# Kernel optimization log

Measured on AMD Instinct MI355X. Metric: run time of the kernel, lower is better.

Reference implementation:

```python
import jax, jax.numpy as jnp
import numpy as np

def setup_inputs() -> dict:
    key = jax.random.key(0)
    k1, k2, k3, k4 = jax.random.split(key, 4)
    B, S, E, H = 4, 4096, 1024, 64
    x = jax.random.normal(k1, (B, S, E), dtype=jnp.float32)
    scale = E ** -0.5  # keep activations well-scaled like trained Linear weights
    Wq = jax.random.normal(k2, (E, H), dtype=jnp.float32) * scale
    Wk = jax.random.normal(k3, (E, H), dtype=jnp.float32) * scale
    Wv = jax.random.normal(k4, (E, H), dtype=jnp.float32) * scale
    return {"x": x, "Wq": Wq, "Wk": Wk, "Wv": Wv}

def reference(x, Wq, Wk, Wv):
    # x: [B, S, E]; W*: [E, H]
    B, S, E = x.shape
    H = Wq.shape[1]
    q = jnp.einsum('bse,eh->bsh', x, Wq)
    k = jnp.einsum('bse,eh->bsh', x, Wk)
    v = jnp.einsum('bse,eh->bsh', x, Wv)
    att = jnp.einsum('bqh,bkh->bqk', q, k) * (H ** -0.5)  # [B, S, S]
    causal = jnp.tril(jnp.ones((S, S), dtype=bool))
    att = jnp.where(causal, att, -jnp.inf)
    att = jax.nn.softmax(att, axis=-1)
    # dropout p=0.0 (eval-mode): identity
    return jnp.einsum('bqk,bkh->bqh', att, v)
```

## Files before the change

kernel.cpp:

```cpp
#include <hip/hip_runtime.h>


using short8 = __attribute__((ext_vector_type(8))) short;
using f32x4  = __attribute__((ext_vector_type(4))) float;

#define MFMA16(A, B, C) __builtin_amdgcn_mfma_f32_16x16x32_bf16((A), (B), (C), 0, 0, 0)

typedef const __attribute__((address_space(1))) void* gas_ptr;
typedef __attribute__((address_space(3))) void*       las_ptr;

__device__ __forceinline__ void gload16(const void* g, void* l) {
    __builtin_amdgcn_global_load_lds((gas_ptr)g, (las_ptr)l, 16, 0, 0);
}

__device__ __forceinline__ unsigned short f2bf(float f) {
    unsigned u = __builtin_bit_cast(unsigned, f);
    u += 0x7fffu + ((u >> 16) & 1u);
    return (unsigned short)(u >> 16);
}
__device__ __forceinline__ float bf2f(unsigned short u) {
    unsigned v = ((unsigned)u) << 16;
    return __builtin_bit_cast(float, v);
}

__device__ __forceinline__ float exp2_fast(float x) {
#if __has_builtin(__builtin_amdgcn_exp2f)
    return __builtin_amdgcn_exp2f(x);
#else
    float r;
    asm("v_exp_f32 %0, %1" : "=v"(r) : "v"(x));
    return r;
#endif
}

__global__ __launch_bounds__(256) void transpose_w(
    const float* __restrict__ Wq,
    const float* __restrict__ Wk,
    const float* __restrict__ Wv,
    unsigned short* __restrict__ Ws)
{
    int o = blockIdx.x * 256 + threadIdx.x;
    if (o < 196608) {
        int j    = o & 7;
        int l    = (o >> 3) & 63;
        int g    = (o >> 9) & 7;
        int rem  = o >> 12;
        int mt   = rem % 3;
        int sk   = rem / 3;
        int c    = g >> 2, nt = g & 3;
        int quad = l >> 4, n  = l & 15;
        int e    = sk * 64 + c * 32 + quad * 8 + j;
        int h    = nt * 16 + n;
        const float* W = (mt == 0) ? Wq : (mt == 1) ? Wk : Wv;
        Ws[o] = f2bf(W[e * 64 + h]);
    }
}

__global__ __launch_bounds__(256, 2) void proj_all(
    const float* __restrict__ x,
    const unsigned short* __restrict__ Ws,
    unsigned short* __restrict__ Qo,
    unsigned short* __restrict__ Ko,
    unsigned short* __restrict__ Vto)
{
    const int m0   = blockIdx.x * 32;
    const int tid  = threadIdx.x;
    const int lane = tid & 63;
    const int wv   = tid >> 6;
    const int rt   = wv & 1;
    const int ch   = wv >> 1;
    const int quad = lane >> 4;
    const int n    = lane & 15;

    __shared__ __align__(16) short wf[2][24][64][8];

    const f32x4 zero4 = {0.f, 0.f, 0.f, 0.f};
    f32x4 acc[3][2];
    #pragma unroll
    for (int mt = 0; mt < 3; ++mt)
        #pragma unroll
        for (int ntl = 0; ntl < 2; ++ntl) acc[mt][ntl] = zero4;

    const float* xrow = x + (size_t)(m0 + rt * 16 + n) * 1024 + 8 * quad;

    auto stageW = [&](int k0, int p) {
        int sk = k0 >> 6;
        #pragma unroll
        for (int it = 0; it < 6; ++it) {
            int f = wv + 4 * it;
            gload16(Ws + (((size_t)sk * 24 + f) << 9) + lane * 8, &wf[p][f][0][0]);
        }
    };

    f32x4 ua[4], ub[4];
    #pragma unroll
    for (int j = 0; j < 4; ++j) {
        const float* s = xrow + ((j & 1) ? 4 : 0) + ((j >> 1) ? 32 : 0);
        ua[j] = *(const f32x4*)s;
    }
    stageW(0, 0);
    __syncthreads();

    auto body = [&](int k0, f32x4 (&uc)[4], f32x4 (&un)[4], int pp) {
        int nk = (k0 < 960) ? k0 + 64 : 0;
        #pragma unroll
        for (int j = 0; j < 4; ++j) {
            const float* s = xrow + nk + ((j & 1) ? 4 : 0) + ((j >> 1) ? 32 : 0);
            un[j] = *(const f32x4*)s;
        }
        if (k0 < 960) stageW(k0 + 64, pp ^ 1);

        short8 a0, a1;
        #pragma unroll
        for (int j = 0; j < 4; ++j) {
            a0[j]     = (short)f2bf(uc[0][j]);
            a0[4 + j] = (short)f2bf(uc[1][j]);
            a1[j]     = (short)f2bf(uc[2][j]);
            a1[4 + j] = (short)f2bf(uc[3][j]);
        }

        #pragma unroll
        for (int mt = 0; mt < 3; ++mt)
            #pragma unroll
            for (int ntl = 0; ntl < 2; ++ntl) {
                int nt = 2 * ch + ntl;
                acc[mt][ntl] = MFMA16(a0, *(const short8*)(&wf[pp][mt * 8 + nt][lane][0]),     acc[mt][ntl]);
                acc[mt][ntl] = MFMA16(a1, *(const short8*)(&wf[pp][mt * 8 + 4 + nt][lane][0]), acc[mt][ntl]);
            }

        __syncthreads();
    };

    for (int k0 = 0; k0 < 1024; k0 += 128) {
        body(k0,      ua, ub, 0);
        body(k0 + 64, ub, ua, 1);
    }

    #pragma unroll
    for (int ntl = 0; ntl < 2; ++ntl) {
        int h = (2 * ch + ntl) * 16 + n;
        #pragma unroll
        for (int r = 0; r < 4; ++r) {
            int m = m0 + rt * 16 + quad * 4 + r;
            Qo[(size_t)m * 64 + h] = f2bf(acc[0][ntl][r]);
            Ko[(size_t)m * 64 + h] = f2bf(acc[1][ntl][r]);
            int b = m >> 12, s2 = m & 4095;
            Vto[((size_t)(b * 80 + h)) * 4096 + s2] = f2bf(acc[2][ntl][r]);
        }
    }
}

template <int SPLIT>
__device__ __forceinline__ void attn_body(
    const unsigned short* __restrict__ Q,
    const unsigned short* __restrict__ K,
    const unsigned short* __restrict__ Vt,
    float* __restrict__ dst,
    int b, int r0, int kt0, int kt1)
{
    const int tid  = threadIdx.x;
    const int lane = tid & 63;
    const int wv   = tid >> 6;
    const int quad = lane >> 4;
    const int n    = lane & 15;
    const int ktmask = r0 >> 6;

    __shared__ __align__(16) short kf[2][8][64][8];
    __shared__ __align__(16) short vf[2][8][64][8];
    __shared__ __align__(16) unsigned short pbuf[4][32][72];

    short8 qa[2][2];
    #pragma unroll
    for (int rg = 0; rg < 2; ++rg) {
        const unsigned short* qp =
            Q + (size_t)(b * 4096 + r0 + wv * 32 + rg * 16 + n) * 64 + quad * 8;
        #pragma unroll
        for (int j = 0; j < 8; ++j) {
            qa[rg][0][j] = (short)f2bf(bf2f(qp[j])      * 0.18033688f);
            qa[rg][1][j] = (short)f2bf(bf2f(qp[32 + j]) * 0.18033688f);
        }
    }

    const f32x4 zero4 = {0.f, 0.f, 0.f, 0.f};
    f32x4 oacc[2][4];
    float lacc[2][4];
    #pragma unroll
    for (int rg = 0; rg < 2; ++rg)
        #pragma unroll
        for (int nt = 0; nt < 4; ++nt) { oacc[rg][nt] = zero4; lacc[rg][nt] = 0.f; }

    const unsigned short* kbase = K  + ((size_t)b * 4096 + n) * 64 + quad * 8;
    const unsigned short* vbase = Vt + ((size_t)b * 80 + n) * 4096 + quad * 8;

    auto stage = [&](int kt, int p) {
        #pragma unroll
        for (int it = 0; it < 4; ++it) {
            int f = wv + 4 * it;
            if (f < 8) {
                int c = f >> 2, nt = f & 3;
                gload16(kbase + (size_t)(kt * 64 + nt * 16) * 64 + c * 32, &kf[p][f][0][0]);
            } else {
                int pnl = f - 8;
                int nt = pnl >> 1, c = pnl & 1;
                gload16(vbase + (size_t)nt * 16 * 4096 + kt * 64 + c * 32, &vf[p][pnl][0][0]);
            }
        }
    };

    int p = 0;
    stage(kt0, 0);
    __syncthreads();

    for (int kt = kt0; kt <= kt1; ++kt) {
        if (kt < kt1) stage(kt + 1, p ^ 1);

        f32x4 sacc[2][4];
        #pragma unroll
        for (int rg = 0; rg < 2; ++rg)
            #pragma unroll
            for (int nt = 0; nt < 4; ++nt) sacc[rg][nt] = zero4;

        __builtin_amdgcn_s_setprio(1);
        #pragma unroll
        for (int nt = 0; nt < 4; ++nt) {
            short8 ka = *(const short8*)(&kf[p][nt][lane][0]);
            short8 kb = *(const short8*)(&kf[p][4 + nt][lane][0]);
            #pragma unroll
            for (int rg = 0; rg < 2; ++rg) {
                sacc[rg][nt] = MFMA16(qa[rg][0], ka, sacc[rg][nt]);
                sacc[rg][nt] = MFMA16(qa[rg][1], kb, sacc[rg][nt]);
            }
        }
        __builtin_amdgcn_s_setprio(0);

        if (kt >= ktmask) {
            #pragma unroll
            for (int rg = 0; rg < 2; ++rg) {
                int qg = r0 + wv * 32 + rg * 16 + quad * 4;
                #pragma unroll
                for (int nt = 0; nt < 4; ++nt)
                    #pragma unroll
                    for (int r = 0; r < 4; ++r) {
                        int key = kt * 64 + nt * 16 + n;
                        if (key > qg + r) sacc[rg][nt][r] = -1e30f;
                    }
            }
        }

        #pragma unroll
        for (int rg = 0; rg < 2; ++rg)
            #pragma unroll
            for (int r = 0; r < 4; ++r) {
                float rs = 0.f;
                #pragma unroll
                for (int nt = 0; nt < 4; ++nt) {
                    unsigned short pv = f2bf(exp2_fast(sacc[rg][nt][r]));
                    pbuf[wv][rg * 16 + quad * 4 + r][nt * 16 + n] = pv;
                    rs += bf2f(pv);
                }
                lacc[rg][r] += rs;
            }

        short8 pa[2][2];
        #pragma unroll
        for (int rg = 0; rg < 2; ++rg) {
            pa[rg][0] = *(const short8*)(&pbuf[wv][rg * 16 + n][quad * 8]);
            pa[rg][1] = *(const short8*)(&pbuf[wv][rg * 16 + n][32 + quad * 8]);
        }
        __builtin_amdgcn_s_setprio(1);
        #pragma unroll
        for (int nt = 0; nt < 4; ++nt) {
            short8 va = *(const short8*)(&vf[p][2 * nt][lane][0]);
            short8 vb = *(const short8*)(&vf[p][2 * nt + 1][lane][0]);
            #pragma unroll
            for (int rg = 0; rg < 2; ++rg) {
                oacc[rg][nt] = MFMA16(pa[rg][0], va, oacc[rg][nt]);
                oacc[rg][nt] = MFMA16(pa[rg][1], vb, oacc[rg][nt]);
            }
        }
        __builtin_amdgcn_s_setprio(0);

        __syncthreads();
        p ^= 1;
    }

    #pragma unroll
    for (int rg = 0; rg < 2; ++rg)
        #pragma unroll
        for (int r = 0; r < 4; ++r) {
            float v = lacc[rg][r];
            v += __shfl_xor(v, 1);
            v += __shfl_xor(v, 2);
            v += __shfl_xor(v, 4);
            v += __shfl_xor(v, 8);
            lacc[rg][r] = v;
        }

    if (SPLIT) {
        #pragma unroll
        for (int rg = 0; rg < 2; ++rg)
            #pragma unroll
            for (int r = 0; r < 4; ++r) {
                int row = wv * 32 + rg * 16 + quad * 4 + r;
                #pragma unroll
                for (int nt = 0; nt < 4; ++nt)
                    dst[row * 64 + nt * 16 + n] = oacc[rg][nt][r];
                if (n == 0) dst[8192 + row] = lacc[rg][r];
            }
    } else {
        #pragma unroll
        for (int rg = 0; rg < 2; ++rg)
            #pragma unroll
            for (int r = 0; r < 4; ++r) {
                float inv = 1.f / lacc[rg][r];
                int q = r0 + wv * 32 + rg * 16 + quad * 4 + r;
                #pragma unroll
                for (int nt = 0; nt < 4; ++nt)
                    dst[(size_t)(b * 4096 + q) * 64 + nt * 16 + n] = oacc[rg][nt][r] * inv;
            }
    }
}

__global__ __launch_bounds__(256, 3) void attn_part(
    const unsigned short* __restrict__ Q,
    const unsigned short* __restrict__ K,
    const unsigned short* __restrict__ Vt,
    float* __restrict__ Part)
{
    int id = blockIdx.x;
    int b  = id & 3;
    int t  = 143 - (id >> 2);
    int g  = 0;
    while (2 * (g + 1) * (g + 2) <= t) ++g;
    int u  = t - 2 * g * (g + 1);
    int qt = 4 * g + u / (g + 1);
    int c  = u - (u / (g + 1)) * (g + 1);

    int r0  = qt * 128;
    int kt0 = c * 8;
    int kt1 = min(kt0 + 7, 2 * qt + 1);

    float* dst = Part + (size_t)(b * 144 + t) * 8320;
    attn_body<1>(Q, K, Vt, dst, b, r0, kt0, kt1);
}

__global__ __launch_bounds__(256, 3) void attn_mono(
    const unsigned short* __restrict__ Q,
    const unsigned short* __restrict__ K,
    const unsigned short* __restrict__ Vt,
    float* __restrict__ out)
{
    int id = blockIdx.x;
    int qt = 31 - (id >> 2);
    int b  = id & 3;
    attn_body<0>(Q, K, Vt, out, b, qt * 128, 0, 2 * qt + 1);
}

__global__ __launch_bounds__(256) void combine(
    const float* __restrict__ Part, float* __restrict__ out)
{
    int id    = blockIdx.x;
    int slice = id & 3;
    int bq    = id >> 2;
    int b     = bq & 3;
    int qt    = bq >> 2;
    int g     = qt >> 2;
    int nc    = g + 1;
    int t0    = 2 * g * (g + 1) + (qt & 3) * (g + 1);
    const float* P0 = Part + (size_t)(b * 144 + t0) * 8320;

    int tid = threadIdx.x;

    __shared__ float invden[32];
    if (tid < 32) {
        float d[8] = {0, 0, 0, 0, 0, 0, 0, 0};
        #pragma unroll 8
        for (int c = 0; c < 8; ++c)
            if (c < nc) d[c] = P0[c * 8320 + 8192 + slice * 32 + tid];
        invden[tid] = 1.f / (((d[0] + d[1]) + (d[2] + d[3])) +
                             ((d[4] + d[5]) + (d[6] + d[7])));
    }

    float acc[8] = {0, 0, 0, 0, 0, 0, 0, 0};
    const float* Pe = P0 + slice * 2048 + tid;
    for (int c = 0; c < nc; ++c) {
        const float* Pc = Pe + (size_t)c * 8320;
        #pragma unroll
        for (int j = 0; j < 8; ++j)
            acc[j] += Pc[j * 256];
    }

    __syncthreads();
    #pragma unroll
    for (int j = 0; j < 8; ++j) {
        int e   = slice * 2048 + j * 256 + tid;
        int row = (e >> 6) & 31;
        out[((size_t)b * 4096 + qt * 128 + slice * 32) * 64 + (size_t)(j * 256 + tid)]
            = acc[j] * invden[row];
    }
}

extern "C" void kernel_launch(void* const* d_in, const int* in_sizes, int n_in,
                              void* d_out, int out_size, void* d_ws, size_t ws_size,
                              hipStream_t stream) {
    const float* x  = (const float*)d_in[0];
    const float* Wq = (const float*)d_in[1];
    const float* Wk = (const float*)d_in[2];
    const float* Wv = (const float*)d_in[3];
    float* outp = (float*)d_out;
    unsigned short* ws = (unsigned short*)d_ws;

    unsigned short* Qw  = ws;
    unsigned short* Kw  = ws + 1048576;
    unsigned short* Vtw = ws + 2097152;
    unsigned short* Wsp = ws + 3407872;

    size_t part_off = ((size_t)3604480 * 2 + 255) & ~(size_t)255;
    size_t need     = part_off + (size_t)4 * 144 * 8320 * 4;
    float* Part = (float*)((char*)d_ws + part_off);

    transpose_w<<<dim3(768), dim3(256), 0, stream>>>(Wq, Wk, Wv, Wsp);
    proj_all<<<dim3(512), dim3(256), 0, stream>>>(x, Wsp, Qw, Kw, Vtw);

    if (ws_size >= need) {
        attn_part<<<dim3(576), dim3(256), 0, stream>>>(Qw, Kw, Vtw, Part);
        combine<<<dim3(512), dim3(256), 0, stream>>>(Part, outp);
    } else {
        attn_mono<<<dim3(128), dim3(256), 0, stream>>>(Qw, Kw, Vtw, outp);
    }
}
```

Baseline: 154.6 us.

## Rework projection to 512-thread direct weight loads, drop setprio, split combine finer

The projection kernel now runs 8 waves per block, each computing one 16-column tile per row group. Weight fragments are read straight from global memory into registers instead of being staged through double-buffered LDS, which removes that LDS traffic and the per-step barriers. The attention kernels drop their s_setprio hints around MFMA sections. The combine kernel splits each query tile into 8 slices instead of 4, doubling its block count for more parallelism. In exchange, weight reads now depend on the caches and are repeated across waves.

```diff
diff --git a/kernel.cpp b/kernel.cpp
--- a/kernel.cpp
+++ b/kernel.cpp
@@ -56,7 +56,7 @@
     }
 }
 
-__global__ __launch_bounds__(256, 2) void proj_all(
+__global__ __launch_bounds__(512, 4) void proj_all(
     const float* __restrict__ x,
     const unsigned short* __restrict__ Ws,
     unsigned short* __restrict__ Qo,
@@ -67,48 +67,37 @@
     const int tid  = threadIdx.x;
     const int lane = tid & 63;
     const int wv   = tid >> 6;
-    const int rt   = wv & 1;
-    const int ch   = wv >> 1;
+    const int rt   = wv >> 2;
+    const int ch   = wv & 3;
     const int quad = lane >> 4;
     const int n    = lane & 15;
 
-    __shared__ __align__(16) short wf[2][24][64][8];
-
     const f32x4 zero4 = {0.f, 0.f, 0.f, 0.f};
-    f32x4 acc[3][2];
-    #pragma unroll
-    for (int mt = 0; mt < 3; ++mt)
-        #pragma unroll
-        for (int ntl = 0; ntl < 2; ++ntl) acc[mt][ntl] = zero4;
+    f32x4 acc[3];
+    acc[0] = zero4; acc[1] = zero4; acc[2] = zero4;
 
     const float* xrow = x + (size_t)(m0 + rt * 16 + n) * 1024 + 8 * quad;
-
-    auto stageW = [&](int k0, int p) {
+    const unsigned short* wbase = Ws + (size_t)lane * 8;
+
+    f32x4 ua[4], ub[4];
+    #pragma unroll
+    for (int j = 0; j < 4; ++j)
+        ua[j] = *(const f32x4*)(xrow + (j & 1) * 4 + (j >> 1) * 32);
+
+    auto body = [&](int k0, f32x4 (&uc)[4], f32x4 (&un)[4]) {
+        int nk = (k0 < 960) ? k0 + 64 : 0;
+        #pragma unroll
+        for (int j = 0; j < 4; ++j)
+            un[j] = *(const f32x4*)(xrow + nk + (j & 1) * 4 + (j >> 1) * 32);
+
         int sk = k0 >> 6;
-        #pragma unroll
-        for (int it = 0; it < 6; ++it) {
-            int f = wv + 4 * it;
-            gload16(Ws + (((size_t)sk * 24 + f) << 9) + lane * 8, &wf[p][f][0][0]);
-        }
-    };
-
-    f32x4 ua[4], ub[4];
-    #pragma unroll
-    for (int j = 0; j < 4; ++j) {
-        const float* s = xrow + ((j & 1) ? 4 : 0) + ((j >> 1) ? 32 : 0);
-        ua[j] = *(const f32x4*)s;
-    }
-    stageW(0, 0);
-    __syncthreads();
-
-    auto body = [&](int k0, f32x4 (&uc)[4], f32x4 (&un)[4], int pp) {
-        int nk = (k0 < 960) ? k0 + 64 : 0;
-        #pragma unroll
-        for (int j = 0; j < 4; ++j) {
-            const float* s = xrow + nk + ((j & 1) ? 4 : 0) + ((j >> 1) ? 32 : 0);
-            un[j] = *(const f32x4*)s;
-        }
-        if (k0 < 960) stageW(k0 + 64, pp ^ 1);
+        const unsigned short* wp = wbase + (size_t)(sk * 24) * 512;
+        short8 wfr[6];
+        #pragma unroll
+        for (int mt = 0; mt < 3; ++mt) {
+            wfr[2 * mt]     = *(const short8*)(wp + (size_t)(mt * 8 + ch) * 512);
+            wfr[2 * mt + 1] = *(const short8*)(wp + (size_t)(mt * 8 + 4 + ch) * 512);
+        }
 
         short8 a0, a1;
         #pragma unroll
@@ -120,33 +109,25 @@
         }
 
         #pragma unroll
-        for (int mt = 0; mt < 3; ++mt)
-            #pragma unroll
-            for (int ntl = 0; ntl < 2; ++ntl) {
-                int nt = 2 * ch + ntl;
-                acc[mt][ntl] = MFMA16(a0, *(const short8*)(&wf[pp][mt * 8 + nt][lane][0]),     acc[mt][ntl]);
-                acc[mt][ntl] = MFMA16(a1, *(const short8*)(&wf[pp][mt * 8 + 4 + nt][lane][0]), acc[mt][ntl]);
-            }
-
-        __syncthreads();
+        for (int mt = 0; mt < 3; ++mt) {
+            acc[mt] = MFMA16(a0, wfr[2 * mt],     acc[mt]);
+            acc[mt] = MFMA16(a1, wfr[2 * mt + 1], acc[mt]);
+        }
     };
 
     for (int k0 = 0; k0 < 1024; k0 += 128) {
-        body(k0,      ua, ub, 0);
-        body(k0 + 64, ub, ua, 1);
-    }
-
-    #pragma unroll
-    for (int ntl = 0; ntl < 2; ++ntl) {
-        int h = (2 * ch + ntl) * 16 + n;
-        #pragma unroll
-        for (int r = 0; r < 4; ++r) {
-            int m = m0 + rt * 16 + quad * 4 + r;
-            Qo[(size_t)m * 64 + h] = f2bf(acc[0][ntl][r]);
-            Ko[(size_t)m * 64 + h] = f2bf(acc[1][ntl][r]);
-            int b = m >> 12, s2 = m & 4095;
-            Vto[((size_t)(b * 80 + h)) * 4096 + s2] = f2bf(acc[2][ntl][r]);
-        }
+        body(k0,      ua, ub);
+        body(k0 + 64, ub, ua);
+    }
+
+    const int h = ch * 16 + n;
+    #pragma unroll
+    for (int r = 0; r < 4; ++r) {
+        int m = m0 + rt * 16 + quad * 4 + r;
+        Qo[(size_t)m * 64 + h] = f2bf(acc[0][r]);
+        Ko[(size_t)m * 64 + h] = f2bf(acc[1][r]);
+        int b = m >> 12, s2 = m & 4095;
+        Vto[((size_t)(b * 80 + h)) * 4096 + s2] = f2bf(acc[2][r]);
     }
 }
 
@@ -220,7 +201,6 @@
             #pragma unroll
             for (int nt = 0; nt < 4; ++nt) sacc[rg][nt] = zero4;
 
-        __builtin_amdgcn_s_setprio(1);
         #pragma unroll
         for (int nt = 0; nt < 4; ++nt) {
             short8 ka = *(const short8*)(&kf[p][nt][lane][0]);
@@ -231,7 +211,6 @@
                 sacc[rg][nt] = MFMA16(qa[rg][1], kb, sacc[rg][nt]);
             }
         }
-        __builtin_amdgcn_s_setprio(0);
 
         if (kt >= ktmask) {
             #pragma unroll
@@ -267,7 +246,6 @@
             pa[rg][0] = *(const short8*)(&pbuf[wv][rg * 16 + n][quad * 8]);
             pa[rg][1] = *(const short8*)(&pbuf[wv][rg * 16 + n][32 + quad * 8]);
         }
-        __builtin_amdgcn_s_setprio(1);
         #pragma unroll
         for (int nt = 0; nt < 4; ++nt) {
             short8 va = *(const short8*)(&vf[p][2 * nt][lane][0]);
@@ -278,7 +256,6 @@
                 oacc[rg][nt] = MFMA16(pa[rg][1], vb, oacc[rg][nt]);
             }
         }
-        __builtin_amdgcn_s_setprio(0);
 
         __syncthreads();
         p ^= 1;
@@ -360,8 +337,8 @@
     const float* __restrict__ Part, float* __restrict__ out)
 {
     int id    = blockIdx.x;
-    int slice = id & 3;
-    int bq    = id >> 2;
+    int slice = id & 7;
+    int bq    = id >> 3;
     int b     = bq & 3;
     int qt    = bq >> 2;
     int g     = qt >> 2;
@@ -371,31 +348,31 @@
 
     int tid = threadIdx.x;
 
-    __shared__ float invden[32];
-    if (tid < 32) {
+    __shared__ float invden[16];
+    if (tid < 16) {
         float d[8] = {0, 0, 0, 0, 0, 0, 0, 0};
         #pragma unroll 8
         for (int c = 0; c < 8; ++c)
-            if (c < nc) d[c] = P0[c * 8320 + 8192 + slice * 32 + tid];
+            if (c < nc) d[c] = P0[c * 8320 + 8192 + slice * 16 + tid];
         invden[tid] = 1.f / (((d[0] + d[1]) + (d[2] + d[3])) +
                              ((d[4] + d[5]) + (d[6] + d[7])));
     }
 
-    float acc[8] = {0, 0, 0, 0, 0, 0, 0, 0};
-    const float* Pe = P0 + slice * 2048 + tid;
+    float acc[4] = {0, 0, 0, 0};
+    const float* Pe = P0 + slice * 1024 + tid;
     for (int c = 0; c < nc; ++c) {
         const float* Pc = Pe + (size_t)c * 8320;
         #pragma unroll
-        for (int j = 0; j < 8; ++j)
+        for (int j = 0; j < 4; ++j)
             acc[j] += Pc[j * 256];
     }
 
     __syncthreads();
     #pragma unroll
-    for (int j = 0; j < 8; ++j) {
-        int e   = slice * 2048 + j * 256 + tid;
-        int row = (e >> 6) & 31;
-        out[((size_t)b * 4096 + qt * 128 + slice * 32) * 64 + (size_t)(j * 256 + tid)]
+    for (int j = 0; j < 4; ++j) {
+        int e   = j * 256 + tid;
+        int row = e >> 6;
+        out[((size_t)b * 4096 + qt * 128 + slice * 16) * 64 + (size_t)e]
             = acc[j] * invden[row];
     }
 }
@@ -420,11 +397,11 @@
     float* Part = (float*)((char*)d_ws + part_off);
 
     transpose_w<<<dim3(768), dim3(256), 0, stream>>>(Wq, Wk, Wv, Wsp);
-    proj_all<<<dim3(512), dim3(256), 0, stream>>>(x, Wsp, Qw, Kw, Vtw);
+    proj_all<<<dim3(512), dim3(512), 0, stream>>>(x, Wsp, Qw, Kw, Vtw);
 
     if (ws_size >= need) {
         attn_part<<<dim3(576), dim3(256), 0, stream>>>(Qw, Kw, Vtw, Part);
-        combine<<<dim3(512), dim3(256), 0, stream>>>(Part, outp);
+        combine<<<dim3(1024), dim3(256), 0, stream>>>(Part, outp);
     } else {
         attn_mono<<<dim3(128), dim3(256), 0, stream>>>(Qw, Kw, Vtw, outp);
     }
```

Result: slower. 168.2 us (+8.8%).

## Triple-buffer x and W via LDS in projection, split combine finer, drop setprio

Applied to the files above, without the earlier changes.

The projection kernel now stages x tiles through LDS with direct global-to-LDS loads, using a swizzled layout and a three-deep buffer with manual vmcnt waits, instead of per-thread register prefetch. This is meant to hide global latency better, at the cost of more LDS and an occupancy hint lowered to 1. The combine kernel is split into 8 slices per tile instead of 4, doubling the block count for more parallelism. The s_setprio hints are removed from the attention loop.

```diff
diff --git a/kernel.cpp b/kernel.cpp
--- a/kernel.cpp
+++ b/kernel.cpp
@@ -56,7 +56,7 @@
     }
 }
 
-__global__ __launch_bounds__(256, 2) void proj_all(
+__global__ __launch_bounds__(256, 1) void proj_all(
     const float* __restrict__ x,
     const unsigned short* __restrict__ Ws,
     unsigned short* __restrict__ Qo,
@@ -72,7 +72,8 @@
     const int quad = lane >> 4;
     const int n    = lane & 15;
 
-    __shared__ __align__(16) short wf[2][24][64][8];
+    __shared__ __align__(16) float xs[3][8][64][4];
+    __shared__ __align__(16) short wf[3][24][64][8];
 
     const f32x4 zero4 = {0.f, 0.f, 0.f, 0.f};
     f32x4 acc[3][2];
@@ -81,60 +82,68 @@
         #pragma unroll
         for (int ntl = 0; ntl < 2; ++ntl) acc[mt][ntl] = zero4;
 
-    const float* xrow = x + (size_t)(m0 + rt * 16 + n) * 1024 + 8 * quad;
-
-    auto stageW = [&](int k0, int p) {
-        int sk = k0 >> 6;
+    auto stage = [&](int t, int qb) {
+        int k0 = t * 64;
+        #pragma unroll
+        for (int it = 0; it < 2; ++it) {
+            int i     = wv + 4 * it;
+            int chunk = n ^ (quad << 2);
+            gload16(x + (size_t)(m0 + 4 * i + quad) * 1024 + k0 + chunk * 4,
+                    &xs[qb][i][0][0]);
+        }
         #pragma unroll
         for (int it = 0; it < 6; ++it) {
             int f = wv + 4 * it;
-            gload16(Ws + (((size_t)sk * 24 + f) << 9) + lane * 8, &wf[p][f][0][0]);
+            gload16(Ws + (((size_t)t * 24 + f) << 9) + lane * 8, &wf[qb][f][0][0]);
         }
     };
 
-    f32x4 ua[4], ub[4];
-    #pragma unroll
-    for (int j = 0; j < 4; ++j) {
-        const float* s = xrow + ((j & 1) ? 4 : 0) + ((j >> 1) ? 32 : 0);
-        ua[j] = *(const f32x4*)s;
-    }
-    stageW(0, 0);
-    __syncthreads();
-
-    auto body = [&](int k0, f32x4 (&uc)[4], f32x4 (&un)[4], int pp) {
-        int nk = (k0 < 960) ? k0 + 64 : 0;
+    auto compute = [&](int qb) {
+        int sub = n & 3, s = sub << 2;
+        const float* xp = &xs[qb][rt * 4 + (n >> 2)][0][0] + sub * 64;
+        f32x4 u0 = *(const f32x4*)(xp + (((2 * quad)     ^ s) << 2));
+        f32x4 u1 = *(const f32x4*)(xp + (((2 * quad + 1) ^ s) << 2));
+        f32x4 u2 = *(const f32x4*)(xp + (((8 + 2 * quad) ^ s) << 2));
+        f32x4 u3 = *(const f32x4*)(xp + (((9 + 2 * quad) ^ s) << 2));
+        short8 a0, a1;
         #pragma unroll
         for (int j = 0; j < 4; ++j) {
-            const float* s = xrow + nk + ((j & 1) ? 4 : 0) + ((j >> 1) ? 32 : 0);
-            un[j] = *(const f32x4*)s;
-        }
-        if (k0 < 960) stageW(k0 + 64, pp ^ 1);
-
-        short8 a0, a1;
-        #pragma unroll
-        for (int j = 0; j < 4; ++j) {
-            a0[j]     = (short)f2bf(uc[0][j]);
-            a0[4 + j] = (short)f2bf(uc[1][j]);
-            a1[j]     = (short)f2bf(uc[2][j]);
-            a1[4 + j] = (short)f2bf(uc[3][j]);
-        }
-
+            a0[j]     = (short)f2bf(u0[j]);
+            a0[4 + j] = (short)f2bf(u1[j]);
+            a1[j]     = (short)f2bf(u2[j]);
+            a1[4 + j] = (short)f2bf(u3[j]);
+        }
         #pragma unroll
         for (int mt = 0; mt < 3; ++mt)
             #pragma unroll
             for (int ntl = 0; ntl < 2; ++ntl) {
                 int nt = 2 * ch + ntl;
-                acc[mt][ntl] = MFMA16(a0, *(const short8*)(&wf[pp][mt * 8 + nt][lane][0]),     acc[mt][ntl]);
-                acc[mt][ntl] = MFMA16(a1, *(const short8*)(&wf[pp][mt * 8 + 4 + nt][lane][0]), acc[mt][ntl]);
-            }
-
-        __syncthreads();
+                acc[mt][ntl] = MFMA16(a0, *(const short8*)(&wf[qb][mt * 8 + nt][lane][0]),     acc[mt][ntl]);
+                acc[mt][ntl] = MFMA16(a1, *(const short8*)(&wf[qb][mt * 8 + 4 + nt][lane][0]), acc[mt][ntl]);
+            }
     };
 
-    for (int k0 = 0; k0 < 1024; k0 += 128) {
-        body(k0,      ua, ub, 0);
-        body(k0 + 64, ub, ua, 1);
-    }
+    stage(0, 0);
+    stage(1, 1);
+
+    int qb = 0;
+    for (int t = 0; t < 15; ++t) {
+        asm volatile("s_waitcnt vmcnt(8)" ::: "memory");
+        asm volatile("s_waitcnt lgkmcnt(0)" ::: "memory");
+        __builtin_amdgcn_s_barrier();
+        __builtin_amdgcn_sched_barrier(0);
+        if (t < 14) {
+            int qn = qb + 2; if (qn >= 3) qn -= 3;
+            stage(t + 2, qn);
+        }
+        compute(qb);
+        if (++qb == 3) qb = 0;
+    }
+    asm volatile("s_waitcnt vmcnt(0)" ::: "memory");
+    asm volatile("s_waitcnt lgkmcnt(0)" ::: "memory");
+    __builtin_amdgcn_s_barrier();
+    __builtin_amdgcn_sched_barrier(0);
+    compute(qb);
 
     #pragma unroll
     for (int ntl = 0; ntl < 2; ++ntl) {
@@ -220,7 +229,6 @@
             #pragma unroll
             for (int nt = 0; nt < 4; ++nt) sacc[rg][nt] = zero4;
 
-        __builtin_amdgcn_s_setprio(1);
         #pragma unroll
         for (int nt = 0; nt < 4; ++nt) {
             short8 ka = *(const short8*)(&kf[p][nt][lane][0]);
@@ -231,7 +239,6 @@
                 sacc[rg][nt] = MFMA16(qa[rg][1], kb, sacc[rg][nt]);
             }
         }
-        __builtin_amdgcn_s_setprio(0);
 
         if (kt >= ktmask) {
             #pragma unroll
@@ -267,7 +274,6 @@
             pa[rg][0] = *(const short8*)(&pbuf[wv][rg * 16 + n][quad * 8]);
             pa[rg][1] = *(const short8*)(&pbuf[wv][rg * 16 + n][32 + quad * 8]);
         }
-        __builtin_amdgcn_s_setprio(1);
         #pragma unroll
         for (int nt = 0; nt < 4; ++nt) {
             short8 va = *(const short8*)(&vf[p][2 * nt][lane][0]);
@@ -278,7 +284,6 @@
                 oacc[rg][nt] = MFMA16(pa[rg][1], vb, oacc[rg][nt]);
             }
         }
-        __builtin_amdgcn_s_setprio(0);
 
         __syncthreads();
         p ^= 1;
@@ -360,8 +365,8 @@
     const float* __restrict__ Part, float* __restrict__ out)
 {
     int id    = blockIdx.x;
-    int slice = id & 3;
-    int bq    = id >> 2;
+    int slice = id & 7;
+    int bq    = id >> 3;
     int b     = bq & 3;
     int qt    = bq >> 2;
     int g     = qt >> 2;
@@ -371,31 +376,31 @@
 
     int tid = threadIdx.x;
 
-    __shared__ float invden[32];
-    if (tid < 32) {
+    __shared__ float invden[16];
+    if (tid < 16) {
         float d[8] = {0, 0, 0, 0, 0, 0, 0, 0};
         #pragma unroll 8
         for (int c = 0; c < 8; ++c)
-            if (c < nc) d[c] = P0[c * 8320 + 8192 + slice * 32 + tid];
+            if (c < nc) d[c] = P0[c * 8320 + 8192 + slice * 16 + tid];
         invden[tid] = 1.f / (((d[0] + d[1]) + (d[2] + d[3])) +
                              ((d[4] + d[5]) + (d[6] + d[7])));
     }
 
-    float acc[8] = {0, 0, 0, 0, 0, 0, 0, 0};
-    const float* Pe = P0 + slice * 2048 + tid;
+    float acc[4] = {0, 0, 0, 0};
+    const float* Pe = P0 + slice * 1024 + tid;
     for (int c = 0; c < nc; ++c) {
         const float* Pc = Pe + (size_t)c * 8320;
         #pragma unroll
-        for (int j = 0; j < 8; ++j)
+        for (int j = 0; j < 4; ++j)
             acc[j] += Pc[j * 256];
     }
 
     __syncthreads();
     #pragma unroll
-    for (int j = 0; j < 8; ++j) {
-        int e   = slice * 2048 + j * 256 + tid;
-        int row = (e >> 6) & 31;
-        out[((size_t)b * 4096 + qt * 128 + slice * 32) * 64 + (size_t)(j * 256 + tid)]
+    for (int j = 0; j < 4; ++j) {
+        int e   = j * 256 + tid;
+        int row = e >> 6;
+        out[((size_t)b * 4096 + qt * 128 + slice * 16) * 64 + (size_t)e]
             = acc[j] * invden[row];
     }
 }
@@ -424,7 +429,7 @@
 
     if (ws_size >= need) {
         attn_part<<<dim3(576), dim3(256), 0, stream>>>(Qw, Kw, Vtw, Part);
-        combine<<<dim3(512), dim3(256), 0, stream>>>(Part, outp);
+        combine<<<dim3(1024), dim3(256), 0, stream>>>(Part, outp);
     } else {
         attn_mono<<<dim3(128), dim3(256), 0, stream>>>(Qw, Kw, Vtw, outp);
     }
```

Measured after the change: 156.1 us. Within noise of the previous version (+0.9%).
